# Optimization experiments

Hardware: AMD Instinct MI355X
Metric: run time of the kernel (lower is better)

Reference implementation:

```python
import jax, jax.numpy as jnp
import numpy as np

N = 2048
DIM = 1024
NH = 16
DK = DIM // NH  # 64

def setup_inputs() -> dict:
    key = jax.random.key(0)
    kx, kq, kk, kv = jax.random.split(key, 4)
    # nn.Linear(dim_in, dim_in, bias=False): init ~ U(-1/sqrt(dim_in), 1/sqrt(dim_in))
    b = 1.0 / np.sqrt(DIM)
    return {
        "x": jax.random.normal(kx, (N, DIM), dtype=jnp.float32),
        "rela": jnp.zeros((1,), dtype=jnp.float32),  # unused by the module
        "Wq": jax.random.uniform(kq, (DIM, DIM), jnp.float32, -b, b),
        "Wk": jax.random.uniform(kk, (DIM, DIM), jnp.float32, -b, b),
        "Wv": jax.random.uniform(kv, (DIM, DIM), jnp.float32, -b, b),
    }

def reference(x, rela, Wq, Wk, Wv):
    n = x.shape[0]
    scale = 1.0 / np.sqrt(DK)
    # torch Linear: x @ W.T ; reshape to [n, nh, dk] then heads first -> [nh, n, dk]
    q = (x @ Wq.T).reshape(n, NH, DK).transpose(1, 0, 2)
    k = (x @ Wk.T).reshape(n, NH, DK).transpose(1, 0, 2)
    v = (x @ Wv.T).reshape(n, NH, DK).transpose(1, 0, 2)
    dist = jnp.einsum('hnd,hmd->hnm', q, k) * scale  # [nh, n, n]
    dist = jax.nn.softmax(dist, axis=-1)
    att = jnp.einsum('hnm,hmd->hnd', dist, v)        # [nh, n, dk]
    return att.transpose(1, 0, 2).reshape(n, DIM)
```

## Files before the change

### kernel.cpp

```cpp
#include <hip/hip_runtime.h>

#define SN 2048
#define SDIM 1024
#define SNH 16
#define SDK 64

typedef short short8 __attribute__((ext_vector_type(8)));
typedef short s16x4 __attribute__((ext_vector_type(4)));
typedef unsigned short u16;
typedef u16 u16x4 __attribute__((ext_vector_type(4)));
typedef unsigned u32x4 __attribute__((ext_vector_type(4)));
typedef float f32x4 __attribute__((ext_vector_type(4)));

__device__ __forceinline__ u16 f2b(float f){
  unsigned u = __builtin_bit_cast(unsigned, f);
  u += 0x7fffu + ((u >> 16) & 1u);
  return (u16)(u >> 16);
}

__device__ __forceinline__ float b2f(u16 b){
  unsigned u = ((unsigned)b) << 16;
  return __builtin_bit_cast(float, u);
}

__device__ __forceinline__ float fast_exp2(float x){
#if __has_builtin(__builtin_amdgcn_exp2f)
  return __builtin_amdgcn_exp2f(x);
#else
  float r; asm("v_exp_f32 %0, %1" : "=v"(r) : "v"(x)); return r;
#endif
}

__device__ __forceinline__ void async_cp16(const void* g, void* l){
  __builtin_amdgcn_global_load_lds(
      (const __attribute__((address_space(1))) unsigned*)g,
      (__attribute__((address_space(3))) unsigned*)l, 16, 0, 0);
}

__global__ void conv_all(const float* __restrict__ x, const float* __restrict__ wq,
                         const float* __restrict__ wk, const float* __restrict__ wv,
                         u16* __restrict__ xb, u16* __restrict__ wb){
  const int NX4 = (SN * SDIM) / 4;
  const int NW4 = (SDIM * SDIM) / 4;
  const int total = NX4 + 3 * NW4;
  int i = blockIdx.x * blockDim.x + threadIdx.x;
  int stride = gridDim.x * blockDim.x;
  for (int idx = i; idx < total; idx += stride){
    const float* src; u16* dst; int off;
    if (idx < NX4){ src = x; dst = xb; off = idx; }
    else {
      int t = idx - NX4; int ws = t >> 18; off = t & (NW4 - 1);
      src = (ws == 0) ? wq : ((ws == 1) ? wk : wv);
      dst = wb + (size_t)ws * SDIM * SDIM;
    }
    float4 v = reinterpret_cast<const float4*>(src)[off];
    u16x4 o = { f2b(v.x), f2b(v.y), f2b(v.z), f2b(v.w) };
    *reinterpret_cast<u16x4*>(&dst[(size_t)off * 4]) = o;
  }
}

__global__ __launch_bounds__(512, 6) void proj_gemm(const u16* __restrict__ xb, const u16* __restrict__ wb,
                                                    u16* __restrict__ qb, u16* __restrict__ kb,
                                                    u16* __restrict__ vtb){
  __shared__ __align__(16) u16 Asm[2][64 * 64];
  __shared__ __align__(16) u16 Bsm[2][128 * 64];
  const int tid = threadIdx.x, w = tid >> 6, lane = tid & 63;
  const int r = lane & 15, hi = lane >> 4;
  const int tm = blockIdx.x * 64, tn = blockIdx.y * 128;
  const int z = blockIdx.z;
  const u16* W = wb + (size_t)z * SDIM * SDIM;
  const int kk = w >> 2;
  const int wr = (w >> 1) & 1, wc = w & 1;
  const int srow = lane >> 3;
  const int schunk = (lane & 7) ^ (lane >> 3);
  f32x4 acc[2][4] = {};

  auto stage = [&](int b, int kt){
    async_cp16(xb + (size_t)(tm + w * 8 + srow) * SDIM + kt + schunk * 8, &Asm[b][w * 8 * 64]);
#pragma unroll
    for (int c = 0; c < 2; c++){
      int row = w * 16 + c * 8;
      async_cp16(W + (size_t)(tn + row + srow) * SDIM + kt + schunk * 8, &Bsm[b][row * 64]);
    }
  };

  stage(0, 0);
  asm volatile("s_waitcnt vmcnt(0)" ::: "memory");
  __builtin_amdgcn_s_barrier();
  __builtin_amdgcn_sched_barrier(0);

  int cur = 0;
  for (int kt = 0; kt < SDIM; kt += 64){
    if (kt + 64 < SDIM) stage(cur ^ 1, kt + 64);
    __builtin_amdgcn_s_setprio(1);
    {
      short8 af[2], bf[4];
      int cc = (kk * 4 + hi) ^ (r & 7);
#pragma unroll
      for (int mr = 0; mr < 2; mr++)
        af[mr] = *reinterpret_cast<const short8*>(&Asm[cur][(wr * 32 + mr * 16 + r) * 64 + cc * 8]);
#pragma unroll
      for (int nr = 0; nr < 4; nr++)
        bf[nr] = *reinterpret_cast<const short8*>(&Bsm[cur][(wc * 64 + nr * 16 + r) * 64 + cc * 8]);
#pragma unroll
      for (int mr = 0; mr < 2; mr++)
#pragma unroll
        for (int nr = 0; nr < 4; nr++)
          acc[mr][nr] = __builtin_amdgcn_mfma_f32_16x16x32_bf16(af[mr], bf[nr], acc[mr][nr], 0, 0, 0);
    }
    __builtin_amdgcn_s_setprio(0);
    asm volatile("s_waitcnt vmcnt(0)" ::: "memory");
    __builtin_amdgcn_s_barrier();
    __builtin_amdgcn_sched_barrier(0);
    cur ^= 1;
  }

  float* scr = reinterpret_cast<float*>(&Bsm[0][0]);
  const int slot = w & 3;
  if (kk == 1){
#pragma unroll
    for (int mr = 0; mr < 2; mr++)
#pragma unroll
      for (int nr = 0; nr < 4; nr++){
        int fid = mr * 4 + nr;
        int a = slot * 2048 + fid * 256 + r * 16 + ((hi + r) & 3) * 4;
        *reinterpret_cast<f32x4*>(&scr[a]) = acc[mr][nr];
      }
  }
  __syncthreads();
  if (kk == 0){
#pragma unroll
    for (int mr = 0; mr < 2; mr++)
#pragma unroll
      for (int nr = 0; nr < 4; nr++){
        int fid = mr * 4 + nr;
        int a = slot * 2048 + fid * 256 + r * 16 + ((hi + r) & 3) * 4;
        f32x4 t = *reinterpret_cast<const f32x4*>(&scr[a]);
        acc[mr][nr][0] += t[0]; acc[mr][nr][1] += t[1];
        acc[mr][nr][2] += t[2]; acc[mr][nr][3] += t[3];
      }

    if (z == 2){
#pragma unroll
      for (int mr = 0; mr < 2; mr++)
#pragma unroll
        for (int nr = 0; nr < 4; nr++){
          u16x4 o4 = { f2b(acc[mr][nr][0]), f2b(acc[mr][nr][1]),
                       f2b(acc[mr][nr][2]), f2b(acc[mr][nr][3]) };
          int col = tn + wc * 64 + nr * 16 + r;
          int row = tm + wr * 32 + mr * 16 + hi * 4;
          *reinterpret_cast<u16x4*>(&vtb[(size_t)col * SN + row]) = o4;
        }
    } else {
      u16* outp = (z == 0) ? qb : kb;
      const float scl = (z == 0) ? 0.18033688011112043f : 1.0f;
#pragma unroll
      for (int mr = 0; mr < 2; mr++)
#pragma unroll
        for (int nr = 0; nr < 4; nr++)
#pragma unroll
          for (int j = 0; j < 4; j++){
            int row = tm + wr * 32 + mr * 16 + hi * 4 + j;
            int col = tn + wc * 64 + nr * 16 + r;
            outp[(size_t)row * SDIM + col] = f2b(acc[mr][nr][j] * scl);
          }
    }
  }
}

__global__ __launch_bounds__(512, 4) void attn(const u16* __restrict__ qb, const u16* __restrict__ kb,
                                               const u16* __restrict__ vtb,
                                               u16* __restrict__ po, float* __restrict__ pl){
  __shared__ __align__(16) u16 klds[2][64 * 64];
  __shared__ __align__(16) u16 vlds[2][64 * 64];
  const int tid = threadIdx.x, w = tid >> 6, lane = tid & 63;
  const int r = lane & 15, hi = lane >> 4;

  int flat = blockIdx.x + 8 * blockIdx.y + 128 * blockIdx.z;
  int sw = (flat & 7) * 64 + (flat >> 3);
  const int q0 = (sw & 7) * 256, h = (sw >> 3) & 15, z = sw >> 7;

  const int srow_off = lane >> 3;
  const int schunk   = (lane & 7) ^ (lane >> 3);

  short8 aq[2][2];
#pragma unroll
  for (int sub = 0; sub < 2; sub++){
    int qrow = q0 + w * 32 + sub * 16 + r;
    aq[sub][0] = *reinterpret_cast<const short8*>(&qb[(size_t)qrow * SDIM + h * SDK + hi * 8]);
    aq[sub][1] = *reinterpret_cast<const short8*>(&qb[(size_t)qrow * SDIM + h * SDK + 32 + hi * 8]);
  }
  f32x4 oacc[2][4] = {};
  float lacc0 = 0.f, lacc1 = 0.f;
  short8 paf0[2], paf1[2];

  auto stageK = [&](int buf, int t){
    int rho = w * 8 + srow_off;
    int kvp = 32 * (rho >> 5) + 8 * ((rho >> 2) & 3) + 4 * ((rho >> 4) & 1) + (rho & 3);
    async_cp16(kb + (size_t)(t + kvp) * SDIM + h * SDK + schunk * 8,
               &klds[buf][(w * 8) * 64]);
  };
  auto stageV = [&](int buf, int t){
    int rho = w * 8 + srow_off;
    async_cp16(vtb + (size_t)(h * SDK + rho) * SN + t + schunk * 8,
               &vlds[buf][(w * 8) * 64]);
  };

  auto QK = [&](const u16* kbuf, f32x4* s0, f32x4* s1){
    __builtin_amdgcn_s_setprio(1);
#pragma unroll
    for (int ct = 0; ct < 4; ct++){
      int row = ct * 16 + r;
      int c0 = hi ^ (r & 7);
      short8 bk0 = *reinterpret_cast<const short8*>(&kbuf[row * 64 + c0 * 8]);
      short8 bk1 = *reinterpret_cast<const short8*>(&kbuf[row * 64 + (c0 ^ 4) * 8]);
      f32x4 zero = {};
      s0[ct] = __builtin_amdgcn_mfma_f32_16x16x32_bf16(bk0, aq[0][0], zero, 0, 0, 0);
      s1[ct] = __builtin_amdgcn_mfma_f32_16x16x32_bf16(bk0, aq[1][0], zero, 0, 0, 0);
      s0[ct] = __builtin_amdgcn_mfma_f32_16x16x32_bf16(bk1, aq[0][1], s0[ct], 0, 0, 0);
      s1[ct] = __builtin_amdgcn_mfma_f32_16x16x32_bf16(bk1, aq[1][1], s1[ct], 0, 0, 0);
    }
    __builtin_amdgcn_s_setprio(0);
  };

  auto EXPPACK = [&](const f32x4* s0, const f32x4* s1){
    uint2 pc0[4], pc1[4];
#pragma unroll
    for (int ct = 0; ct < 4; ct++){
      float a0 = fast_exp2(s0[ct][0]), a1 = fast_exp2(s0[ct][1]);
      float a2 = fast_exp2(s0[ct][2]), a3 = fast_exp2(s0[ct][3]);
      lacc0 += (a0 + a1) + (a2 + a3);
      pc0[ct].x = (__builtin_bit_cast(unsigned, a0) >> 16) |
                  (__builtin_bit_cast(unsigned, a1) & 0xffff0000u);
      pc0[ct].y = (__builtin_bit_cast(unsigned, a2) >> 16) |
                  (__builtin_bit_cast(unsigned, a3) & 0xffff0000u);
      float b0 = fast_exp2(s1[ct][0]), b1 = fast_exp2(s1[ct][1]);
      float b2 = fast_exp2(s1[ct][2]), b3 = fast_exp2(s1[ct][3]);
      lacc1 += (b0 + b1) + (b2 + b3);
      pc1[ct].x = (__builtin_bit_cast(unsigned, b0) >> 16) |
                  (__builtin_bit_cast(unsigned, b1) & 0xffff0000u);
      pc1[ct].y = (__builtin_bit_cast(unsigned, b2) >> 16) |
                  (__builtin_bit_cast(unsigned, b3) & 0xffff0000u);
    }
#pragma unroll
    for (int c = 0; c < 2; c++){
      u32x4 u0 = { pc0[2*c].x, pc0[2*c].y, pc0[2*c+1].x, pc0[2*c+1].y };
      u32x4 u1 = { pc1[2*c].x, pc1[2*c].y, pc1[2*c+1].x, pc1[2*c+1].y };
      paf0[c] = __builtin_bit_cast(short8, u0);
      paf1[c] = __builtin_bit_cast(short8, u1);
    }
  };

  auto PV = [&](const u16* vbuf){
    __builtin_amdgcn_s_setprio(1);
#pragma unroll
    for (int dt = 0; dt < 4; dt++){
      int row = dt * 16 + r;
      int swz = row & 7;
      short8 bvc[2];
#pragma unroll
      for (int c = 0; c < 2; c++)
        bvc[c] = *reinterpret_cast<const short8*>(&vbuf[row * 64 + ((4 * c + hi) ^ swz) * 8]);
#pragma unroll
      for (int c = 0; c < 2; c++){
        oacc[0][dt] = __builtin_amdgcn_mfma_f32_16x16x32_bf16(paf0[c], bvc[c], oacc[0][dt], 0, 0, 0);
        oacc[1][dt] = __builtin_amdgcn_mfma_f32_16x16x32_bf16(paf1[c], bvc[c], oacc[1][dt], 0, 0, 0);
      }
    }
    __builtin_amdgcn_s_setprio(0);
  };

  const int t0 = z * (SN / 4);
  const int NT = (SN / 4) / 64;

  stageK(0, t0); stageV(0, t0); stageK(1, t0 + 64);
  asm volatile("s_waitcnt vmcnt(0)" ::: "memory");
  __builtin_amdgcn_s_barrier();
  __builtin_amdgcn_sched_barrier(0);
  {
    f32x4 s0[4], s1[4];
    QK(&klds[0][0], s0, s1);
    EXPPACK(s0, s1);
  }
  __builtin_amdgcn_s_barrier();
  __builtin_amdgcn_sched_barrier(0);

  for (int it = 0; it < NT; ++it){
    const int cur = it & 1;
    const int t = t0 + it * 64;
    const bool hasN1 = (it + 1 < NT), hasN2 = (it + 2 < NT);
    if (hasN1) stageV(cur ^ 1, t + 64);
    if (hasN2) stageK(cur, t + 128);
    f32x4 s0[4], s1[4];
    if (hasN1) QK(&klds[cur ^ 1][0], s0, s1);
    PV(&vlds[cur][0]);
    if (hasN1) EXPPACK(s0, s1);
    asm volatile("s_waitcnt vmcnt(0)" ::: "memory");
    __builtin_amdgcn_s_barrier();
    __builtin_amdgcn_sched_barrier(0);
  }

  lacc0 += __shfl_xor(lacc0, 16); lacc0 += __shfl_xor(lacc0, 32);
  lacc1 += __shfl_xor(lacc1, 16); lacc1 += __shfl_xor(lacc1, 32);

  const size_t zh = (size_t)z * SNH + h;
#pragma unroll
  for (int sub = 0; sub < 2; sub++)
#pragma unroll
    for (int dt = 0; dt < 4; dt++)
#pragma unroll
      for (int j = 0; j < 4; j++){
        int row = q0 + w * 32 + sub * 16 + hi * 4 + j;
        po[(zh * SN + row) * SDK + dt * 16 + r] = f2b(oacc[sub][dt][j]);
      }
  if (hi == 0){
    pl[zh * SN + q0 + w * 32 + r] = lacc0;
    pl[zh * SN + q0 + w * 32 + 16 + r] = lacc1;
  }
}

__global__ void merge(const u16* __restrict__ po, const float* __restrict__ pl,
                      float* __restrict__ out){
  int gid = blockIdx.x * blockDim.x + threadIdx.x;
  int c4 = gid & 15;
  int rowid = gid >> 4;
  int h = rowid & 15, q = rowid >> 4;
  float L = 0.f;
  float4 o = { 0.f, 0.f, 0.f, 0.f };
#pragma unroll
  for (int z = 0; z < 4; z++){
    size_t zh = (size_t)z * SNH + h;
    L += pl[zh * SN + q];
    u16x4 a = *reinterpret_cast<const u16x4*>(&po[(zh * SN + q) * SDK + c4 * 4]);
    o.x += b2f(a[0]); o.y += b2f(a[1]); o.z += b2f(a[2]); o.w += b2f(a[3]);
  }
  float rL = 1.0f / L;
  o.x *= rL; o.y *= rL; o.z *= rL; o.w *= rL;
  reinterpret_cast<float4*>(&out[(size_t)q * SDIM + h * SDK])[c4] = o;
}

extern "C" void kernel_launch(void* const* d_in, const int* in_sizes, int n_in,
                              void* d_out, int out_size, void* d_ws, size_t ws_size,
                              hipStream_t stream){
  const float* x  = (const float*)d_in[0];
  const float* Wq = (const float*)d_in[2];
  const float* Wk = (const float*)d_in[3];
  const float* Wv = (const float*)d_in[4];
  float* out = (float*)d_out;

  char* ws = (char*)d_ws;
  u16* xb  = (u16*)(ws);
  u16* wb  = (u16*)(ws + (4  << 20));
  u16* qb  = (u16*)(ws + (10 << 20));
  u16* kb  = (u16*)(ws + (14 << 20));
  u16* vtb = (u16*)(ws + (18 << 20));
  u16* po  = (u16*)(ws + (22 << 20));
  float* pl = (float*)(ws + (38 << 20));

  conv_all<<<2048, 256, 0, stream>>>(x, Wq, Wk, Wv, xb, wb);

  dim3 pg(SN / 64, SDIM / 128, 3);
  proj_gemm<<<pg, 512, 0, stream>>>(xb, wb, qb, kb, vtb);

  dim3 ag(SN / 256, SNH, 4);
  attn<<<ag, 512, 0, stream>>>(qb, kb, vtb, po, pl);

  merge<<<(SN * SNH * 16) / 256, 256, 0, stream>>>(po, pl, out);
}
```

Baseline: 57.26 us.

## Split attention KV range into six uneven chunks and widen merge loads

The attention kernel's KV split goes from 4 equal chunks of 8 tiles to 6 uneven chunks (6,6,5,5,5,5 tiles), which gives 768 blocks instead of 512 and raises the launch-bounds occupancy hint to 6 blocks per CU. This should fill the CUs better and shorten each block's serial loop. The block-index swizzle is reworked for the larger grid, the bf16 packing uses a byte-permute builtin, and merge reads 8 bf16 values per thread across the 6 partials. In exchange, the partial buffers and the merge reduction grow, and the tighter register budget under the new launch bounds could cause spills.

Measured after the change: 167.9 us. 193% more time.

```diff
diff --git a/kernel.cpp b/kernel.cpp
--- a/kernel.cpp
+++ b/kernel.cpp
@@ -4,11 +4,13 @@
 #define SDIM 1024
 #define SNH 16
 #define SDK 64
+#define NZ 6
 
 typedef short short8 __attribute__((ext_vector_type(8)));
 typedef short s16x4 __attribute__((ext_vector_type(4)));
 typedef unsigned short u16;
 typedef u16 u16x4 __attribute__((ext_vector_type(4)));
+typedef u16 u16x8 __attribute__((ext_vector_type(8)));
 typedef unsigned u32x4 __attribute__((ext_vector_type(4)));
 typedef float f32x4 __attribute__((ext_vector_type(4)));
 
@@ -28,6 +30,16 @@
   return __builtin_amdgcn_exp2f(x);
 #else
   float r; asm("v_exp_f32 %0, %1" : "=v"(r) : "v"(x)); return r;
+#endif
+}
+
+__device__ __forceinline__ unsigned packbf(float lo, float hi){
+  unsigned a = __builtin_bit_cast(unsigned, lo);
+  unsigned b = __builtin_bit_cast(unsigned, hi);
+#if __has_builtin(__builtin_amdgcn_perm)
+  return __builtin_amdgcn_perm(b, a, 0x07060302u);
+#else
+  return (a >> 16) | (b & 0xffff0000u);
 #endif
 }
 
@@ -168,7 +180,7 @@
   }
 }
 
-__global__ __launch_bounds__(512, 4) void attn(const u16* __restrict__ qb, const u16* __restrict__ kb,
+__global__ __launch_bounds__(512, 6) void attn(const u16* __restrict__ qb, const u16* __restrict__ kb,
                                                const u16* __restrict__ vtb,
                                                u16* __restrict__ po, float* __restrict__ pl){
   __shared__ __align__(16) u16 klds[2][64 * 64];
@@ -177,8 +189,11 @@
   const int r = lane & 15, hi = lane >> 4;
 
   int flat = blockIdx.x + 8 * blockIdx.y + 128 * blockIdx.z;
-  int sw = (flat & 7) * 64 + (flat >> 3);
-  const int q0 = (sw & 7) * 256, h = (sw >> 3) & 15, z = sw >> 7;
+  int sw = (flat & 7) * 96 + (flat >> 3);
+  const int h = sw & 15;
+  int rest = sw >> 4;
+  const int q0 = (rest & 7) * 256;
+  const int z = rest >> 3;
 
   const int srow_off = lane >> 3;
   const int schunk   = (lane & 7) ^ (lane >> 3);
@@ -230,17 +245,13 @@
       float a0 = fast_exp2(s0[ct][0]), a1 = fast_exp2(s0[ct][1]);
       float a2 = fast_exp2(s0[ct][2]), a3 = fast_exp2(s0[ct][3]);
       lacc0 += (a0 + a1) + (a2 + a3);
-      pc0[ct].x = (__builtin_bit_cast(unsigned, a0) >> 16) |
-                  (__builtin_bit_cast(unsigned, a1) & 0xffff0000u);
-      pc0[ct].y = (__builtin_bit_cast(unsigned, a2) >> 16) |
-                  (__builtin_bit_cast(unsigned, a3) & 0xffff0000u);
+      pc0[ct].x = packbf(a0, a1);
+      pc0[ct].y = packbf(a2, a3);
       float b0 = fast_exp2(s1[ct][0]), b1 = fast_exp2(s1[ct][1]);
       float b2 = fast_exp2(s1[ct][2]), b3 = fast_exp2(s1[ct][3]);
       lacc1 += (b0 + b1) + (b2 + b3);
-      pc1[ct].x = (__builtin_bit_cast(unsigned, b0) >> 16) |
-                  (__builtin_bit_cast(unsigned, b1) & 0xffff0000u);
-      pc1[ct].y = (__builtin_bit_cast(unsigned, b2) >> 16) |
-                  (__builtin_bit_cast(unsigned, b3) & 0xffff0000u);
+      pc1[ct].x = packbf(b0, b1);
+      pc1[ct].y = packbf(b2, b3);
     }
 #pragma unroll
     for (int c = 0; c < 2; c++){
@@ -270,8 +281,8 @@
     __builtin_amdgcn_s_setprio(0);
   };
 
-  const int t0 = z * (SN / 4);
-  const int NT = (SN / 4) / 64;
+  const int NT = (z < 2) ? 6 : 5;
+  const int t0 = ((z <= 2) ? z * 6 : 12 + (z - 2) * 5) * 64;
 
   stageK(0, t0); stageV(0, t0); stageK(1, t0 + 64);
   asm volatile("s_waitcnt vmcnt(0)" ::: "memory");
@@ -322,21 +333,25 @@
 __global__ void merge(const u16* __restrict__ po, const float* __restrict__ pl,
                       float* __restrict__ out){
   int gid = blockIdx.x * blockDim.x + threadIdx.x;
-  int c4 = gid & 15;
-  int rowid = gid >> 4;
+  int c8 = gid & 7;
+  int rowid = gid >> 3;
   int h = rowid & 15, q = rowid >> 4;
   float L = 0.f;
-  float4 o = { 0.f, 0.f, 0.f, 0.f };
-#pragma unroll
-  for (int z = 0; z < 4; z++){
+  float o[8] = {};
+#pragma unroll
+  for (int z = 0; z < NZ; z++){
     size_t zh = (size_t)z * SNH + h;
     L += pl[zh * SN + q];
-    u16x4 a = *reinterpret_cast<const u16x4*>(&po[(zh * SN + q) * SDK + c4 * 4]);
-    o.x += b2f(a[0]); o.y += b2f(a[1]); o.z += b2f(a[2]); o.w += b2f(a[3]);
+    u16x8 a = *reinterpret_cast<const u16x8*>(&po[(zh * SN + q) * SDK + c8 * 8]);
+#pragma unroll
+    for (int e = 0; e < 8; e++) o[e] += b2f(a[e]);
   }
   float rL = 1.0f / L;
-  o.x *= rL; o.y *= rL; o.z *= rL; o.w *= rL;
-  reinterpret_cast<float4*>(&out[(size_t)q * SDIM + h * SDK])[c4] = o;
+  float4 o0 = { o[0] * rL, o[1] * rL, o[2] * rL, o[3] * rL };
+  float4 o1 = { o[4] * rL, o[5] * rL, o[6] * rL, o[7] * rL };
+  float* dst = &out[(size_t)q * SDIM + h * SDK + c8 * 8];
+  *reinterpret_cast<float4*>(dst) = o0;
+  *reinterpret_cast<float4*>(dst + 4) = o1;
 }
 
 extern "C" void kernel_launch(void* const* d_in, const int* in_sizes, int n_in,
@@ -355,15 +370,15 @@
   u16* kb  = (u16*)(ws + (14 << 20));
   u16* vtb = (u16*)(ws + (18 << 20));
   u16* po  = (u16*)(ws + (22 << 20));
-  float* pl = (float*)(ws + (38 << 20));
+  float* pl = (float*)(ws + (48 << 20));
 
   conv_all<<<2048, 256, 0, stream>>>(x, Wq, Wk, Wv, xb, wb);
 
   dim3 pg(SN / 64, SDIM / 128, 3);
   proj_gemm<<<pg, 512, 0, stream>>>(xb, wb, qb, kb, vtb);
 
-  dim3 ag(SN / 256, SNH, 4);
+  dim3 ag(SN / 256, SNH, NZ);
   attn<<<ag, 512, 0, stream>>>(qb, kb, vtb, po, pl);
 
-  merge<<<(SN * SNH * 16) / 256, 256, 0, stream>>>(po, pl, out);
-}
+  merge<<<(SN * SNH * 8) / 256, 256, 0, stream>>>(po, pl, out);
+}
```
